# Kernel optimization log

Hardware: AMD Instinct MI355X
Metric: run time of the kernel (lower is better)

## Reference

```python
import jax, jax.numpy as jnp
import numpy as np


def _eta(pos, conj):
    # e[0] = pos[:,1::2] repeated into even/odd cols; e[1] = (+/-)pos[:,0::2] likewise
    c = jnp.repeat(pos[:, 1::2], 2, axis=1)
    s = jnp.repeat(pos[:, 0::2], 2, axis=1)
    return jnp.stack([c, s if conj else -s])  # [2, N, d]


def setup_inputs() -> dict:
    key = jax.random.key(0)
    ks = jax.random.split(key, 8)
    B, N, d, H = 8, 4096, 128, 4
    s = 0.02
    return {
        "x": jax.random.normal(ks[0], (B, N, d), jnp.float32),
        "pos": jax.random.normal(ks[1], (N, d), jnp.float32),
        "W_lt": jax.random.normal(ks[2], (d, d), jnp.float32) * s,
        "W_phi": jax.random.normal(ks[3], (d * H, d), jnp.float32) * s,
        "b_phi": jnp.zeros((d * H,), jnp.float32),
        "W_c1": jax.random.normal(ks[4], (H, H), jnp.float32) * s,
        "b_c1": jnp.zeros((H,), jnp.float32),
        "W_c2": jax.random.normal(ks[5], (1, H), jnp.float32) * s,
        "b_c2": jnp.zeros((1,), jnp.float32),
        "ln_g": jnp.ones((d,), jnp.float32),
        "ln_b": jnp.zeros((d,), jnp.float32),
        "W_f1": jax.random.normal(ks[6], (d, d), jnp.float32) * s,
        "b_f1": jnp.zeros((d,), jnp.float32),
        "W_f2": jax.random.normal(ks[7], (d, d), jnp.float32) * s,
        "b_f2": jnp.zeros((d,), jnp.float32),
    }


def reference(x, pos, W_lt, W_phi, b_phi, W_c1, b_c1, W_c2, b_c2,
              ln_g, ln_b, W_f1, b_f1, W_f2, b_f2):
    B, N, d = x.shape
    H = W_phi.shape[0] // d
    x = x @ W_lt.T                                   # linear_trans (no bias)
    e = _eta(pos, False)                             # [2,N,d]
    xe = x[None] * e[:, None]                        # [2,B,N,d]
    # A = ones(N,N) - I  =>  A @ v == sum over nodes minus self
    f = xe.sum(axis=2, keepdims=True) - xe           # [2,B,N,d]
    f_norm = jnp.sqrt(f[0] ** 2 + f[1] ** 2)         # [B,N,d]
    phi = ((x + pos[None]) @ W_phi.T + b_phi).reshape(B, N, H, d)
    # ReLU1(|f| - phi): relu(min(1, f_norm - phi))
    res = jax.nn.relu(jnp.minimum(1.0, f_norm[:, :, None, :] - phi))  # [B,N,H,d]
    ce = _eta(pos, True)
    fec = f[0] * ce[0][None] - f[1] * ce[1][None]    # [B,N,d]
    rfe = res * fec[:, :, None, :]                   # [B,N,H,d]
    # inverse transform: (1/N) * (M @ A) with A symmetric => sum-minus-self over node dim
    inv = (rfe.sum(axis=1, keepdims=True) - rfe) / N  # [B,N,H,d]
    t = inv.transpose(0, 1, 3, 2)                    # [B,N,d,H]
    comb = (jax.nn.relu(t @ W_c1.T + b_c1) @ W_c2.T + b_c2)[..., 0]  # [B,N,d]
    m = x + comb
    mu = m.mean(-1, keepdims=True)
    var = ((m - mu) ** 2).mean(-1, keepdims=True)
    mn = (m - mu) * jax.lax.rsqrt(var + 1e-6) * ln_g + ln_b
    return jax.nn.relu(mn @ W_f1.T + b_f1) @ W_f2.T + b_f2
```

## Files before the change

kernel.cpp:

```cpp
#include <hip/hip_runtime.h>
#include <hip/hip_bf16.h>
#include <hip/hip_fp8.h>


#define DEV __device__ __forceinline__

typedef __attribute__((ext_vector_type(8))) short bf16x8;
typedef __attribute__((ext_vector_type(4))) float f32x4;

constexpr int Bb = 8, Nn = 4096;
constexpr int BN = Bb * Nn;
constexpr int LDP = 136;
constexpr int P8  = 144;

union U8 { ushort u[8]; uint4 v; };

static DEV ushort f2bf(float f) {
    __hip_bfloat16 h = __float2bfloat16(f);
    return *reinterpret_cast<unsigned short*>(&h);
}
static DEV float bf2f(ushort u) {
    return __bfloat162float(*reinterpret_cast<const __hip_bfloat16*>(&u));
}
static DEV unsigned char f2fp8(float f) {
    __hip_fp8_e4m3 q(f);
    return q.__x;
}
static DEV float fp82f(unsigned char u) {
    __hip_fp8_e4m3 q;
    q.__x = u;
    return (float)q;
}

template <int MODE>
__global__ __launch_bounds__(256) void k_mfma_gemm(
    const void* __restrict__ Xv, const float* __restrict__ W,
    const float* __restrict__ bias, const float* __restrict__ pos,
    ushort* __restrict__ outB, unsigned char* __restrict__ out8)
{
    __shared__ __align__(16) ushort xs[64 * LDP];
    __shared__ __align__(16) ushort wsl[128 * LDP];
    const int t = threadIdx.x;
    const int row0 = blockIdx.x * 64;
    const int jt = (MODE == 1) ? blockIdx.y : 0;

    if (MODE == 0) {
        const float* X = (const float*)Xv;
        #pragma unroll
        for (int i = 0; i < 4; ++i) {
            int e = t + i * 256, r = e >> 4, c = (e & 15) * 8;
            const float* p = X + (size_t)(row0 + r) * 128 + c;
            float4 a = *reinterpret_cast<const float4*>(p);
            float4 b = *reinterpret_cast<const float4*>(p + 4);
            U8 u;
            u.u[0] = f2bf(a.x); u.u[1] = f2bf(a.y); u.u[2] = f2bf(a.z); u.u[3] = f2bf(a.w);
            u.u[4] = f2bf(b.x); u.u[5] = f2bf(b.y); u.u[6] = f2bf(b.z); u.u[7] = f2bf(b.w);
            *reinterpret_cast<uint4*>(xs + r * LDP + c) = u.v;
        }
    } else {
        const ushort* X = (const ushort*)Xv;
        #pragma unroll
        for (int i = 0; i < 4; ++i) {
            int e = t + i * 256, r = e >> 4, c = (e & 15) * 8;
            U8 u;
            u.v = *reinterpret_cast<const uint4*>(X + (size_t)(row0 + r) * 128 + c);
            int n = (row0 + r) & (Nn - 1);
            const float* q = pos + (size_t)n * 128 + c;
            float4 pa = *reinterpret_cast<const float4*>(q);
            float4 pb = *reinterpret_cast<const float4*>(q + 4);
            u.u[0] = f2bf(bf2f(u.u[0]) + pa.x);
            u.u[1] = f2bf(bf2f(u.u[1]) + pa.y);
            u.u[2] = f2bf(bf2f(u.u[2]) + pa.z);
            u.u[3] = f2bf(bf2f(u.u[3]) + pa.w);
            u.u[4] = f2bf(bf2f(u.u[4]) + pb.x);
            u.u[5] = f2bf(bf2f(u.u[5]) + pb.y);
            u.u[6] = f2bf(bf2f(u.u[6]) + pb.z);
            u.u[7] = f2bf(bf2f(u.u[7]) + pb.w);
            *reinterpret_cast<uint4*>(xs + r * LDP + c) = u.v;
        }
    }
    {
        const float* Wt = W + (size_t)jt * 128 * 128;
        #pragma unroll
        for (int i = 0; i < 8; ++i) {
            int e = t + i * 256, r = e >> 4, c = (e & 15) * 8;
            const float* p = Wt + (size_t)r * 128 + c;
            float4 a = *reinterpret_cast<const float4*>(p);
            float4 b = *reinterpret_cast<const float4*>(p + 4);
            U8 u;
            u.u[0] = f2bf(a.x); u.u[1] = f2bf(a.y); u.u[2] = f2bf(a.z); u.u[3] = f2bf(a.w);
            u.u[4] = f2bf(b.x); u.u[5] = f2bf(b.y); u.u[6] = f2bf(b.z); u.u[7] = f2bf(b.w);
            *reinterpret_cast<uint4*>(wsl + r * LDP + c) = u.v;
        }
    }
    __syncthreads();

    const int w = t >> 6, l = t & 63;
    const int lr = l & 15;
    const int lk = (l >> 4) * 8;

    f32x4 acc[8];
    #pragma unroll
    for (int cf = 0; cf < 8; ++cf) acc[cf] = f32x4{0.f, 0.f, 0.f, 0.f};

    #pragma unroll
    for (int ks = 0; ks < 4; ++ks) {
        bf16x8 a = *reinterpret_cast<const bf16x8*>(xs + (w * 16 + lr) * LDP + ks * 32 + lk);
        #pragma unroll
        for (int cf = 0; cf < 8; ++cf) {
            bf16x8 b = *reinterpret_cast<const bf16x8*>(wsl + (cf * 16 + lr) * LDP + ks * 32 + lk);
            acc[cf] = __builtin_amdgcn_mfma_f32_16x16x32_bf16(a, b, acc[cf], 0, 0, 0);
        }
    }

    __syncthreads();

    if (MODE == 0) {
        #pragma unroll
        for (int cf = 0; cf < 8; ++cf) {
            int col = cf * 16 + lr;
            #pragma unroll
            for (int reg = 0; reg < 4; ++reg) {
                int rl = w * 16 + (l >> 4) * 4 + reg;
                xs[rl * LDP + col] = f2bf(acc[cf][reg]);
            }
        }
        __syncthreads();
        #pragma unroll
        for (int i = 0; i < 4; ++i) {
            int e = t + i * 256, r = e >> 4, c = (e & 15) * 8;
            uint4 v = *reinterpret_cast<const uint4*>(xs + r * LDP + c);
            *reinterpret_cast<uint4*>(outB + (size_t)(row0 + r) * 128 + c) = v;
        }
    } else {
        unsigned char* x8 = reinterpret_cast<unsigned char*>(xs);
        #pragma unroll
        for (int cf = 0; cf < 8; ++cf) {
            int col = cf * 16 + lr;
            float bv = bias[jt * 128 + col];
            #pragma unroll
            for (int reg = 0; reg < 4; ++reg) {
                int rl = w * 16 + (l >> 4) * 4 + reg;
                x8[rl * P8 + col] = f2fp8(acc[cf][reg] + bv);
            }
        }
        __syncthreads();
        #pragma unroll
        for (int i = 0; i < 2; ++i) {
            int e = t + i * 256, r = e >> 3, c = (e & 7) * 16;
            uint4 v = *reinterpret_cast<const uint4*>(x8 + r * P8 + c);
            *reinterpret_cast<uint4*>(out8 + (size_t)(row0 + r) * 512 + jt * 128 + c) = v;
        }
    }
}

__global__ __launch_bounds__(256) void k_reduceS(
    const ushort* __restrict__ x1b, const float* __restrict__ pos,
    float* __restrict__ PS)
{
    int b = blockIdx.x >> 6, c64 = blockIdx.x & 63;
    int rr = threadIdx.x >> 5, d0 = (threadIdx.x & 31) * 4;
    float a0[4] = {0,0,0,0}, a1[4] = {0,0,0,0};
    #pragma unroll
    for (int i = 0; i < 8; ++i) {
        int n = c64 * 64 + i * 8 + rr;
        size_t r = (size_t)b * Nn + n;
        ushort4 xv = *reinterpret_cast<const ushort4*>(x1b + r * 128 + d0);
        float4 p = *reinterpret_cast<const float4*>(pos + (size_t)n * 128 + d0);
        float x0 = bf2f(xv.x), x1 = bf2f(xv.y), x2 = bf2f(xv.z), x3 = bf2f(xv.w);
        a0[0] += x0 * p.y; a1[0] += x0 * p.x;
        a0[1] += x1 * p.y; a1[1] += x1 * p.x;
        a0[2] += x2 * p.w; a1[2] += x2 * p.z;
        a0[3] += x3 * p.w; a1[3] += x3 * p.z;
    }
    __shared__ float redA[8][128], redB[8][128];
    #pragma unroll
    for (int j = 0; j < 4; ++j) { redA[rr][d0 + j] = a0[j]; redB[rr][d0 + j] = a1[j]; }
    __syncthreads();
    int tt = threadIdx.x;
    float s = 0.f;
    if (tt < 128) {
        #pragma unroll
        for (int k = 0; k < 8; ++k) s += redA[k][tt];
    } else {
        #pragma unroll
        for (int k = 0; k < 8; ++k) s += redB[k][tt - 128];
    }
    PS[(size_t)blockIdx.x * 256 + tt] = s;
}

__global__ __launch_bounds__(256) void k_finS(
    const float* __restrict__ PS, float* __restrict__ S0, float* __restrict__ S1)
{
    int b = blockIdx.x, t = threadIdx.x;
    float s = 0.f;
    #pragma unroll 8
    for (int c = 0; c < 64; ++c) s += PS[(size_t)(b * 64 + c) * 256 + t];
    if (t < 128) S0[b * 128 + t] = s;
    else         S1[b * 128 + (t - 128)] = s;
}

__global__ __launch_bounds__(256) void k_reduceT(
    const ushort* __restrict__ x1b, const unsigned char* __restrict__ phi8,
    const float* __restrict__ pos, const float* __restrict__ S0,
    const float* __restrict__ S1, float* __restrict__ PT)
{
    int b = blockIdx.x >> 6, c64 = blockIdx.x & 63;
    int rr = threadIdx.x >> 5, d0 = (threadIdx.x & 31) * 4;
    float4 S0v = *reinterpret_cast<const float4*>(S0 + b * 128 + d0);
    float4 S1v = *reinterpret_cast<const float4*>(S1 + b * 128 + d0);
    float S0a[4] = {S0v.x, S0v.y, S0v.z, S0v.w};
    float S1a[4] = {S1v.x, S1v.y, S1v.z, S1v.w};
    float acc[4][4];
    #pragma unroll
    for (int h = 0; h < 4; ++h)
        #pragma unroll
        for (int j = 0; j < 4; ++j) acc[h][j] = 0.f;

    #pragma unroll 2
    for (int i = 0; i < 8; ++i) {
        int n = c64 * 64 + i * 8 + rr;
        size_t r = (size_t)b * Nn + n;
        ushort4 xv4 = *reinterpret_cast<const ushort4*>(x1b + r * 128 + d0);
        float4 p = *reinterpret_cast<const float4*>(pos + (size_t)n * 128 + d0);
        float xv[4] = {bf2f(xv4.x), bf2f(xv4.y), bf2f(xv4.z), bf2f(xv4.w)};
        float cc[4] = {p.y, p.y, p.w, p.w};
        float ss[4] = {p.x, p.x, p.z, p.z};
        float fec[4], fn[4];
        #pragma unroll
        for (int j = 0; j < 4; ++j) {
            float f0 = S0a[j] - xv[j] * cc[j];
            float f1 = xv[j] * ss[j] - S1a[j];
            fn[j] = sqrtf(f0 * f0 + f1 * f1);
            fec[j] = f0 * cc[j] - f1 * ss[j];
        }
        #pragma unroll
        for (int h = 0; h < 4; ++h) {
            uchar4 ph4 = *reinterpret_cast<const uchar4*>(phi8 + r * 512 + h * 128 + d0);
            float ph[4] = {fp82f(ph4.x), fp82f(ph4.y), fp82f(ph4.z), fp82f(ph4.w)};
            #pragma unroll
            for (int j = 0; j < 4; ++j)
                acc[h][j] += fmaxf(0.f, fminf(1.f, fn[j] - ph[j])) * fec[j];
        }
    }
    __shared__ float red[8][512];
    #pragma unroll
    for (int h = 0; h < 4; ++h)
        #pragma unroll
        for (int j = 0; j < 4; ++j) red[rr][h * 128 + d0 + j] = acc[h][j];
    __syncthreads();
    int tt = threadIdx.x;
    #pragma unroll
    for (int q = 0; q < 2; ++q) {
        int idx = tt + q * 256;
        float s = 0.f;
        #pragma unroll
        for (int k = 0; k < 8; ++k) s += red[k][idx];
        PT[(size_t)blockIdx.x * 512 + idx] = s;
    }
}

__global__ __launch_bounds__(256) void k_finT(
    const float* __restrict__ PT, float* __restrict__ T)
{
    int idx = blockIdx.x * 256 + threadIdx.x;
    int b = idx >> 9, lo = idx & 511;
    float s = 0.f;
    #pragma unroll 8
    for (int c = 0; c < 64; ++c) s += PT[(size_t)b * 32768 + c * 512 + lo];
    T[idx] = s;
}

__global__ __launch_bounds__(256) void k_comb_ffn(
    const ushort* __restrict__ x1b, const unsigned char* __restrict__ phi8,
    const float* __restrict__ pos, const float* __restrict__ S0,
    const float* __restrict__ S1, const float* __restrict__ T,
    const float* __restrict__ Wc1, const float* __restrict__ bc1,
    const float* __restrict__ Wc2, const float* __restrict__ bc2,
    const float* __restrict__ lng, const float* __restrict__ lnb,
    const float* __restrict__ Wf1, const float* __restrict__ bf1,
    const float* __restrict__ Wf2, const float* __restrict__ bf2,
    float* __restrict__ out)
{
    __shared__ __align__(16) ushort xs[64 * LDP];
    __shared__ __align__(16) ushort wsl[128 * LDP];
    const int t = threadIdx.x;
    const int row0 = blockIdx.x * 64;
    const int w = t >> 6, l = t & 63;

    #pragma unroll
    for (int i = 0; i < 8; ++i) {
        int e = t + i * 256, r = e >> 4, c = (e & 15) * 8;
        const float* p = Wf1 + (size_t)r * 128 + c;
        float4 a = *reinterpret_cast<const float4*>(p);
        float4 b = *reinterpret_cast<const float4*>(p + 4);
        U8 u;
        u.u[0] = f2bf(a.x); u.u[1] = f2bf(a.y); u.u[2] = f2bf(a.z); u.u[3] = f2bf(a.w);
        u.u[4] = f2bf(b.x); u.u[5] = f2bf(b.y); u.u[6] = f2bf(b.z); u.u[7] = f2bf(b.w);
        *reinterpret_cast<uint4*>(wsl + r * LDP + c) = u.v;
    }

    {
        const int d0 = 2 * l;
        const float g0 = lng[d0], g1 = lng[d0 + 1];
        const float be0 = lnb[d0], be1 = lnb[d0 + 1];
        const float c20 = Wc2[0], c21 = Wc2[1], c22 = Wc2[2], c23 = Wc2[3];
        const float b2v = bc2[0];
        for (int i = 0; i < 16; ++i) {
            int rl = w * 16 + i;
            int rrow = row0 + rl;
            int b = rrow >> 12;
            int n = rrow & 4095;
            size_t r = (size_t)rrow;

            ushort2 xv2 = *reinterpret_cast<const ushort2*>(x1b + r * 128 + d0);
            float2 p2 = *reinterpret_cast<const float2*>(pos + (size_t)n * 128 + d0);
            float2 s0 = *reinterpret_cast<const float2*>(S0 + b * 128 + d0);
            float2 s1 = *reinterpret_cast<const float2*>(S1 + b * 128 + d0);
            float cc = p2.y, ss = p2.x;
            float xv[2] = {bf2f(xv2.x), bf2f(xv2.y)};
            float S0a[2] = {s0.x, s0.y}, S1a[2] = {s1.x, s1.y};
            float2 Tv[4];
            #pragma unroll
            for (int h = 0; h < 4; ++h)
                Tv[h] = *reinterpret_cast<const float2*>(T + (b * 4 + h) * 128 + d0);
            uchar2 ph2[4];
            #pragma unroll
            for (int h = 0; h < 4; ++h)
                ph2[h] = *reinterpret_cast<const uchar2*>(phi8 + r * 512 + h * 128 + d0);

            float m[2];
            #pragma unroll
            for (int q = 0; q < 2; ++q) {
                float f0 = S0a[q] - xv[q] * cc;
                float f1 = xv[q] * ss - S1a[q];
                float fn = sqrtf(f0 * f0 + f1 * f1);
                float fec = f0 * cc - f1 * ss;
                float inv[4];
                #pragma unroll
                for (int h = 0; h < 4; ++h) {
                    float ph = fp82f(q ? ph2[h].y : ph2[h].x);
                    float res = fmaxf(0.f, fminf(1.f, fn - ph));
                    float tv = q ? Tv[h].y : Tv[h].x;
                    inv[h] = (tv - res * fec) * (1.f / (float)Nn);
                }
                float comb = b2v;
                float wc2a[4] = {c20, c21, c22, c23};
                #pragma unroll
                for (int h = 0; h < 4; ++h) {
                    float u = bc1[h];
                    #pragma unroll
                    for (int h2 = 0; h2 < 4; ++h2) u += Wc1[h * 4 + h2] * inv[h2];
                    comb += fmaxf(u, 0.f) * wc2a[h];
                }
                m[q] = xv[q] + comb;
            }

            float s = m[0] + m[1];
            #pragma unroll
            for (int off = 32; off; off >>= 1) s += __shfl_xor(s, off);
            float mu = s * (1.f / 128.f);
            float e0 = m[0] - mu, e1 = m[1] - mu;
            float v = e0 * e0 + e1 * e1;
            #pragma unroll
            for (int off = 32; off; off >>= 1) v += __shfl_xor(v, off);
            float rstd = rsqrtf(v * (1.f / 128.f) + 1e-6f);
            ushort2 o;
            o.x = f2bf(e0 * rstd * g0 + be0);
            o.y = f2bf(e1 * rstd * g1 + be1);
            *reinterpret_cast<ushort2*>(xs + rl * LDP + d0) = o;
        }
    }
    __syncthreads();

    const int lr = l & 15;
    const int lk = (l >> 4) * 8;

    f32x4 acc[8];
    #pragma unroll
    for (int cf = 0; cf < 8; ++cf) acc[cf] = f32x4{0.f, 0.f, 0.f, 0.f};
    #pragma unroll
    for (int ks = 0; ks < 4; ++ks) {
        bf16x8 a = *reinterpret_cast<const bf16x8*>(xs + (w * 16 + lr) * LDP + ks * 32 + lk);
        #pragma unroll
        for (int cf = 0; cf < 8; ++cf) {
            bf16x8 b = *reinterpret_cast<const bf16x8*>(wsl + (cf * 16 + lr) * LDP + ks * 32 + lk);
            acc[cf] = __builtin_amdgcn_mfma_f32_16x16x32_bf16(a, b, acc[cf], 0, 0, 0);
        }
    }
    __syncthreads();

    #pragma unroll
    for (int cf = 0; cf < 8; ++cf) {
        int col = cf * 16 + lr;
        float bv = bf1[col];
        #pragma unroll
        for (int reg = 0; reg < 4; ++reg) {
            int rl = w * 16 + (l >> 4) * 4 + reg;
            xs[rl * LDP + col] = f2bf(fmaxf(acc[cf][reg] + bv, 0.f));
        }
    }
    #pragma unroll
    for (int i = 0; i < 8; ++i) {
        int e = t + i * 256, r = e >> 4, c = (e & 15) * 8;
        const float* p = Wf2 + (size_t)r * 128 + c;
        float4 a = *reinterpret_cast<const float4*>(p);
        float4 b = *reinterpret_cast<const float4*>(p + 4);
        U8 u;
        u.u[0] = f2bf(a.x); u.u[1] = f2bf(a.y); u.u[2] = f2bf(a.z); u.u[3] = f2bf(a.w);
        u.u[4] = f2bf(b.x); u.u[5] = f2bf(b.y); u.u[6] = f2bf(b.z); u.u[7] = f2bf(b.w);
        *reinterpret_cast<uint4*>(wsl + r * LDP + c) = u.v;
    }
    __syncthreads();

    #pragma unroll
    for (int cf = 0; cf < 8; ++cf) acc[cf] = f32x4{0.f, 0.f, 0.f, 0.f};
    #pragma unroll
    for (int ks = 0; ks < 4; ++ks) {
        bf16x8 a = *reinterpret_cast<const bf16x8*>(xs + (w * 16 + lr) * LDP + ks * 32 + lk);
        #pragma unroll
        for (int cf = 0; cf < 8; ++cf) {
            bf16x8 b = *reinterpret_cast<const bf16x8*>(wsl + (cf * 16 + lr) * LDP + ks * 32 + lk);
            acc[cf] = __builtin_amdgcn_mfma_f32_16x16x32_bf16(a, b, acc[cf], 0, 0, 0);
        }
    }
    #pragma unroll
    for (int cf = 0; cf < 8; ++cf) {
        int col = cf * 16 + lr;
        float bv = bf2[col];
        #pragma unroll
        for (int reg = 0; reg < 4; ++reg) {
            int r = row0 + w * 16 + (l >> 4) * 4 + reg;
            out[(size_t)r * 128 + col] = acc[cf][reg] + bv;
        }
    }
}

extern "C" void kernel_launch(void* const* d_in, const int* in_sizes, int n_in,
                              void* d_out, int out_size, void* d_ws, size_t ws_size,
                              hipStream_t stream)
{
    const float* x    = (const float*)d_in[0];
    const float* pos  = (const float*)d_in[1];
    const float* Wlt  = (const float*)d_in[2];
    const float* Wphi = (const float*)d_in[3];
    const float* bphi = (const float*)d_in[4];
    const float* Wc1  = (const float*)d_in[5];
    const float* bc1  = (const float*)d_in[6];
    const float* Wc2  = (const float*)d_in[7];
    const float* bc2  = (const float*)d_in[8];
    const float* lng  = (const float*)d_in[9];
    const float* lnb  = (const float*)d_in[10];
    const float* Wf1  = (const float*)d_in[11];
    const float* bf1  = (const float*)d_in[12];
    const float* Wf2  = (const float*)d_in[13];
    const float* bf2  = (const float*)d_in[14];

    float* ws = (float*)d_ws;
    ushort* x1b = (ushort*)ws;
    float* S0   = ws + 2097152;
    float* S1   = S0 + 1024;
    float* T    = S1 + 1024;
    float* PS   = T + 4096;
    float* PT   = PS + 131072;
    unsigned char* phi8 = (unsigned char*)(ws + 2496512);
    float* out  = (float*)d_out;

    k_mfma_gemm<0><<<dim3(BN / 64), 256, 0, stream>>>(x, Wlt, nullptr, pos, x1b, nullptr);
    k_reduceS<<<dim3(512), 256, 0, stream>>>(x1b, pos, PS);
    k_finS<<<dim3(Bb), 256, 0, stream>>>(PS, S0, S1);
    k_mfma_gemm<1><<<dim3(BN / 64, 4), 256, 0, stream>>>(x1b, Wphi, bphi, pos, nullptr, phi8);
    k_reduceT<<<dim3(512), 256, 0, stream>>>(x1b, phi8, pos, S0, S1, PT);
    k_finT<<<dim3(16), 256, 0, stream>>>(PT, T);
    k_comb_ffn<<<dim3(BN / 64), 256, 0, stream>>>(x1b, phi8, pos, S0, S1, T,
                                                  Wc1, bc1, Wc2, bc2, lng, lnb,
                                                  Wf1, bf1, Wf2, bf2, out);
}
```

Baseline: 73.61 us.

## Fuse S-reduction into first GEMM and loop phi GEMM over head tiles

Merges the partial S reduction into the first GEMM's epilogue so x1b is reduced straight from LDS instead of being re-read from global memory, which removes one kernel launch. The phi GEMM now loops over the four 128-column weight tiles inside one block, so the x+pos tile is loaded and converted once rather than four times. The store of each fp8 tile overlaps with loading the next weight tile. FP8 conversions switch from the hip_fp8 header to the raw cvt builtins. In exchange, the grid for the phi GEMM shrinks 4x, with 512 blocks that each run a serial loop, and the partial-sum grid changes from 512 to 512 blocks with a different row grouping. Both could lower parallelism and occupancy because the kernels now use more LDS.

```diff
diff --git a/kernel.cpp b/kernel.cpp
--- a/kernel.cpp
+++ b/kernel.cpp
@@ -1,6 +1,5 @@
 #include <hip/hip_runtime.h>
 #include <hip/hip_bf16.h>
-#include <hip/hip_fp8.h>
 
 
 #define DEV __device__ __forceinline__
@@ -23,75 +22,42 @@
     return __bfloat162float(*reinterpret_cast<const __hip_bfloat16*>(&u));
 }
 static DEV unsigned char f2fp8(float f) {
-    __hip_fp8_e4m3 q(f);
-    return q.__x;
-}
-static DEV float fp82f(unsigned char u) {
-    __hip_fp8_e4m3 q;
-    q.__x = u;
-    return (float)q;
-}
-
-template <int MODE>
-__global__ __launch_bounds__(256) void k_mfma_gemm(
-    const void* __restrict__ Xv, const float* __restrict__ W,
-    const float* __restrict__ bias, const float* __restrict__ pos,
-    ushort* __restrict__ outB, unsigned char* __restrict__ out8)
+    return (unsigned char)(__builtin_amdgcn_cvt_pk_fp8_f32(f, f, 0u, false) & 0xff);
+}
+static DEV float fp8lo(unsigned int u, int) ;
+
+__global__ __launch_bounds__(256) void k_gemm0(
+    const float* __restrict__ X, const float* __restrict__ W,
+    const float* __restrict__ pos, ushort* __restrict__ x1b,
+    float* __restrict__ PS)
 {
     __shared__ __align__(16) ushort xs[64 * LDP];
     __shared__ __align__(16) ushort wsl[128 * LDP];
+    __shared__ float red[4][2][128];
     const int t = threadIdx.x;
     const int row0 = blockIdx.x * 64;
-    const int jt = (MODE == 1) ? blockIdx.y : 0;
-
-    if (MODE == 0) {
-        const float* X = (const float*)Xv;
-        #pragma unroll
-        for (int i = 0; i < 4; ++i) {
-            int e = t + i * 256, r = e >> 4, c = (e & 15) * 8;
-            const float* p = X + (size_t)(row0 + r) * 128 + c;
-            float4 a = *reinterpret_cast<const float4*>(p);
-            float4 b = *reinterpret_cast<const float4*>(p + 4);
-            U8 u;
-            u.u[0] = f2bf(a.x); u.u[1] = f2bf(a.y); u.u[2] = f2bf(a.z); u.u[3] = f2bf(a.w);
-            u.u[4] = f2bf(b.x); u.u[5] = f2bf(b.y); u.u[6] = f2bf(b.z); u.u[7] = f2bf(b.w);
-            *reinterpret_cast<uint4*>(xs + r * LDP + c) = u.v;
-        }
-    } else {
-        const ushort* X = (const ushort*)Xv;
-        #pragma unroll
-        for (int i = 0; i < 4; ++i) {
-            int e = t + i * 256, r = e >> 4, c = (e & 15) * 8;
-            U8 u;
-            u.v = *reinterpret_cast<const uint4*>(X + (size_t)(row0 + r) * 128 + c);
-            int n = (row0 + r) & (Nn - 1);
-            const float* q = pos + (size_t)n * 128 + c;
-            float4 pa = *reinterpret_cast<const float4*>(q);
-            float4 pb = *reinterpret_cast<const float4*>(q + 4);
-            u.u[0] = f2bf(bf2f(u.u[0]) + pa.x);
-            u.u[1] = f2bf(bf2f(u.u[1]) + pa.y);
-            u.u[2] = f2bf(bf2f(u.u[2]) + pa.z);
-            u.u[3] = f2bf(bf2f(u.u[3]) + pa.w);
-            u.u[4] = f2bf(bf2f(u.u[4]) + pb.x);
-            u.u[5] = f2bf(bf2f(u.u[5]) + pb.y);
-            u.u[6] = f2bf(bf2f(u.u[6]) + pb.z);
-            u.u[7] = f2bf(bf2f(u.u[7]) + pb.w);
-            *reinterpret_cast<uint4*>(xs + r * LDP + c) = u.v;
-        }
-    }
-    {
-        const float* Wt = W + (size_t)jt * 128 * 128;
-        #pragma unroll
-        for (int i = 0; i < 8; ++i) {
-            int e = t + i * 256, r = e >> 4, c = (e & 15) * 8;
-            const float* p = Wt + (size_t)r * 128 + c;
-            float4 a = *reinterpret_cast<const float4*>(p);
-            float4 b = *reinterpret_cast<const float4*>(p + 4);
-            U8 u;
-            u.u[0] = f2bf(a.x); u.u[1] = f2bf(a.y); u.u[2] = f2bf(a.z); u.u[3] = f2bf(a.w);
-            u.u[4] = f2bf(b.x); u.u[5] = f2bf(b.y); u.u[6] = f2bf(b.z); u.u[7] = f2bf(b.w);
-            *reinterpret_cast<uint4*>(wsl + r * LDP + c) = u.v;
-        }
+
+    #pragma unroll
+    for (int i = 0; i < 4; ++i) {
+        int e = t + i * 256, r = e >> 4, c = (e & 15) * 8;
+        const float* p = X + (size_t)(row0 + r) * 128 + c;
+        float4 a = *reinterpret_cast<const float4*>(p);
+        float4 b = *reinterpret_cast<const float4*>(p + 4);
+        U8 u;
+        u.u[0] = f2bf(a.x); u.u[1] = f2bf(a.y); u.u[2] = f2bf(a.z); u.u[3] = f2bf(a.w);
+        u.u[4] = f2bf(b.x); u.u[5] = f2bf(b.y); u.u[6] = f2bf(b.z); u.u[7] = f2bf(b.w);
+        *reinterpret_cast<uint4*>(xs + r * LDP + c) = u.v;
+    }
+    #pragma unroll
+    for (int i = 0; i < 8; ++i) {
+        int e = t + i * 256, r = e >> 4, c = (e & 15) * 8;
+        const float* p = W + (size_t)r * 128 + c;
+        float4 a = *reinterpret_cast<const float4*>(p);
+        float4 b = *reinterpret_cast<const float4*>(p + 4);
+        U8 u;
+        u.u[0] = f2bf(a.x); u.u[1] = f2bf(a.y); u.u[2] = f2bf(a.z); u.u[3] = f2bf(a.w);
+        u.u[4] = f2bf(b.x); u.u[5] = f2bf(b.y); u.u[6] = f2bf(b.z); u.u[7] = f2bf(b.w);
+        *reinterpret_cast<uint4*>(wsl + r * LDP + c) = u.v;
     }
     __syncthreads();
 
@@ -102,7 +68,6 @@
     f32x4 acc[8];
     #pragma unroll
     for (int cf = 0; cf < 8; ++cf) acc[cf] = f32x4{0.f, 0.f, 0.f, 0.f};
-
     #pragma unroll
     for (int ks = 0; ks < 4; ++ks) {
         bf16x8 a = *reinterpret_cast<const bf16x8*>(xs + (w * 16 + lr) * LDP + ks * 32 + lk);
@@ -112,81 +77,49 @@
             acc[cf] = __builtin_amdgcn_mfma_f32_16x16x32_bf16(a, b, acc[cf], 0, 0, 0);
         }
     }
-
-    __syncthreads();
-
-    if (MODE == 0) {
-        #pragma unroll
-        for (int cf = 0; cf < 8; ++cf) {
-            int col = cf * 16 + lr;
-            #pragma unroll
-            for (int reg = 0; reg < 4; ++reg) {
-                int rl = w * 16 + (l >> 4) * 4 + reg;
-                xs[rl * LDP + col] = f2bf(acc[cf][reg]);
-            }
-        }
-        __syncthreads();
-        #pragma unroll
-        for (int i = 0; i < 4; ++i) {
-            int e = t + i * 256, r = e >> 4, c = (e & 15) * 8;
-            uint4 v = *reinterpret_cast<const uint4*>(xs + r * LDP + c);
-            *reinterpret_cast<uint4*>(outB + (size_t)(row0 + r) * 128 + c) = v;
-        }
-    } else {
-        unsigned char* x8 = reinterpret_cast<unsigned char*>(xs);
-        #pragma unroll
-        for (int cf = 0; cf < 8; ++cf) {
-            int col = cf * 16 + lr;
-            float bv = bias[jt * 128 + col];
-            #pragma unroll
-            for (int reg = 0; reg < 4; ++reg) {
-                int rl = w * 16 + (l >> 4) * 4 + reg;
-                x8[rl * P8 + col] = f2fp8(acc[cf][reg] + bv);
-            }
-        }
-        __syncthreads();
-        #pragma unroll
-        for (int i = 0; i < 2; ++i) {
-            int e = t + i * 256, r = e >> 3, c = (e & 7) * 16;
-            uint4 v = *reinterpret_cast<const uint4*>(x8 + r * P8 + c);
-            *reinterpret_cast<uint4*>(out8 + (size_t)(row0 + r) * 512 + jt * 128 + c) = v;
-        }
-    }
-}
-
-__global__ __launch_bounds__(256) void k_reduceS(
-    const ushort* __restrict__ x1b, const float* __restrict__ pos,
-    float* __restrict__ PS)
-{
-    int b = blockIdx.x >> 6, c64 = blockIdx.x & 63;
-    int rr = threadIdx.x >> 5, d0 = (threadIdx.x & 31) * 4;
-    float a0[4] = {0,0,0,0}, a1[4] = {0,0,0,0};
-    #pragma unroll
-    for (int i = 0; i < 8; ++i) {
-        int n = c64 * 64 + i * 8 + rr;
-        size_t r = (size_t)b * Nn + n;
-        ushort4 xv = *reinterpret_cast<const ushort4*>(x1b + r * 128 + d0);
-        float4 p = *reinterpret_cast<const float4*>(pos + (size_t)n * 128 + d0);
-        float x0 = bf2f(xv.x), x1 = bf2f(xv.y), x2 = bf2f(xv.z), x3 = bf2f(xv.w);
-        a0[0] += x0 * p.y; a1[0] += x0 * p.x;
-        a0[1] += x1 * p.y; a1[1] += x1 * p.x;
-        a0[2] += x2 * p.w; a1[2] += x2 * p.z;
-        a0[3] += x3 * p.w; a1[3] += x3 * p.z;
-    }
-    __shared__ float redA[8][128], redB[8][128];
-    #pragma unroll
-    for (int j = 0; j < 4; ++j) { redA[rr][d0 + j] = a0[j]; redB[rr][d0 + j] = a1[j]; }
-    __syncthreads();
-    int tt = threadIdx.x;
-    float s = 0.f;
-    if (tt < 128) {
-        #pragma unroll
-        for (int k = 0; k < 8; ++k) s += redA[k][tt];
-    } else {
-        #pragma unroll
-        for (int k = 0; k < 8; ++k) s += redB[k][tt - 128];
-    }
-    PS[(size_t)blockIdx.x * 256 + tt] = s;
+    __syncthreads();
+
+    #pragma unroll
+    for (int cf = 0; cf < 8; ++cf) {
+        int col = cf * 16 + lr;
+        #pragma unroll
+        for (int reg = 0; reg < 4; ++reg) {
+            int rl = w * 16 + (l >> 4) * 4 + reg;
+            xs[rl * LDP + col] = f2bf(acc[cf][reg]);
+        }
+    }
+    __syncthreads();
+
+    #pragma unroll
+    for (int i = 0; i < 4; ++i) {
+        int e = t + i * 256, r = e >> 4, c = (e & 15) * 8;
+        uint4 v = *reinterpret_cast<const uint4*>(xs + r * LDP + c);
+        *reinterpret_cast<uint4*>(x1b + (size_t)(row0 + r) * 128 + c) = v;
+    }
+
+    {
+        int c2 = t & 63, g = t >> 6;
+        float a0e = 0.f, a1e = 0.f, a0o = 0.f, a1o = 0.f;
+        #pragma unroll 4
+        for (int i = 0; i < 16; ++i) {
+            int r = g * 16 + i;
+            int n = (row0 + r) & (Nn - 1);
+            unsigned int v = *reinterpret_cast<const unsigned int*>(xs + r * LDP + 2 * c2);
+            float lo = bf2f((ushort)(v & 0xffff));
+            float hi = bf2f((ushort)(v >> 16));
+            float2 p = *reinterpret_cast<const float2*>(pos + (size_t)n * 128 + 2 * c2);
+            a0e += lo * p.y; a1e += lo * p.x;
+            a0o += hi * p.y; a1o += hi * p.x;
+        }
+        red[g][0][2 * c2] = a0e; red[g][0][2 * c2 + 1] = a0o;
+        red[g][1][2 * c2] = a1e; red[g][1][2 * c2 + 1] = a1o;
+    }
+    __syncthreads();
+    {
+        int half = t >> 7, col = t & 127;
+        float s = red[0][half][col] + red[1][half][col] + red[2][half][col] + red[3][half][col];
+        PS[(size_t)blockIdx.x * 256 + t] = s;
+    }
 }
 
 __global__ __launch_bounds__(256) void k_finS(
@@ -198,6 +131,98 @@
     for (int c = 0; c < 64; ++c) s += PS[(size_t)(b * 64 + c) * 256 + t];
     if (t < 128) S0[b * 128 + t] = s;
     else         S1[b * 128 + (t - 128)] = s;
+}
+
+__global__ __launch_bounds__(256) void k_gemm_phi(
+    const ushort* __restrict__ x1b, const float* __restrict__ W,
+    const float* __restrict__ bias, const float* __restrict__ pos,
+    unsigned char* __restrict__ phi8)
+{
+    __shared__ __align__(16) ushort xs[64 * LDP];
+    __shared__ __align__(16) ushort wsl[128 * LDP];
+    __shared__ __align__(16) unsigned char p8[64 * P8];
+    const int t = threadIdx.x;
+    const int row0 = blockIdx.x * 64;
+    const int w = t >> 6, l = t & 63;
+    const int lr = l & 15;
+    const int lk = (l >> 4) * 8;
+
+    #pragma unroll
+    for (int i = 0; i < 4; ++i) {
+        int e = t + i * 256, r = e >> 4, c = (e & 15) * 8;
+        U8 u;
+        u.v = *reinterpret_cast<const uint4*>(x1b + (size_t)(row0 + r) * 128 + c);
+        int n = (row0 + r) & (Nn - 1);
+        const float* q = pos + (size_t)n * 128 + c;
+        float4 pa = *reinterpret_cast<const float4*>(q);
+        float4 pb = *reinterpret_cast<const float4*>(q + 4);
+        u.u[0] = f2bf(bf2f(u.u[0]) + pa.x);
+        u.u[1] = f2bf(bf2f(u.u[1]) + pa.y);
+        u.u[2] = f2bf(bf2f(u.u[2]) + pa.z);
+        u.u[3] = f2bf(bf2f(u.u[3]) + pa.w);
+        u.u[4] = f2bf(bf2f(u.u[4]) + pb.x);
+        u.u[5] = f2bf(bf2f(u.u[5]) + pb.y);
+        u.u[6] = f2bf(bf2f(u.u[6]) + pb.z);
+        u.u[7] = f2bf(bf2f(u.u[7]) + pb.w);
+        *reinterpret_cast<uint4*>(xs + r * LDP + c) = u.v;
+    }
+
+    for (int jt = 0; jt < 4; ++jt) {
+        __syncthreads();
+        {
+            const float* Wt = W + (size_t)jt * 128 * 128;
+            #pragma unroll
+            for (int i = 0; i < 8; ++i) {
+                int e = t + i * 256, r = e >> 4, c = (e & 15) * 8;
+                const float* p = Wt + (size_t)r * 128 + c;
+                float4 a = *reinterpret_cast<const float4*>(p);
+                float4 b = *reinterpret_cast<const float4*>(p + 4);
+                U8 u;
+                u.u[0] = f2bf(a.x); u.u[1] = f2bf(a.y); u.u[2] = f2bf(a.z); u.u[3] = f2bf(a.w);
+                u.u[4] = f2bf(b.x); u.u[5] = f2bf(b.y); u.u[6] = f2bf(b.z); u.u[7] = f2bf(b.w);
+                *reinterpret_cast<uint4*>(wsl + r * LDP + c) = u.v;
+            }
+            if (jt > 0) {
+                #pragma unroll
+                for (int i = 0; i < 2; ++i) {
+                    int e = t + i * 256, r = e >> 3, c = (e & 7) * 16;
+                    uint4 v = *reinterpret_cast<const uint4*>(p8 + r * P8 + c);
+                    *reinterpret_cast<uint4*>(phi8 + (size_t)(row0 + r) * 512 + (jt - 1) * 128 + c) = v;
+                }
+            }
+        }
+        __syncthreads();
+
+        f32x4 acc[8];
+        #pragma unroll
+        for (int cf = 0; cf < 8; ++cf) acc[cf] = f32x4{0.f, 0.f, 0.f, 0.f};
+        #pragma unroll
+        for (int ks = 0; ks < 4; ++ks) {
+            bf16x8 a = *reinterpret_cast<const bf16x8*>(xs + (w * 16 + lr) * LDP + ks * 32 + lk);
+            #pragma unroll
+            for (int cf = 0; cf < 8; ++cf) {
+                bf16x8 b = *reinterpret_cast<const bf16x8*>(wsl + (cf * 16 + lr) * LDP + ks * 32 + lk);
+                acc[cf] = __builtin_amdgcn_mfma_f32_16x16x32_bf16(a, b, acc[cf], 0, 0, 0);
+            }
+        }
+        #pragma unroll
+        for (int cf = 0; cf < 8; ++cf) {
+            int col = cf * 16 + lr;
+            float bv = bias[jt * 128 + col];
+            #pragma unroll
+            for (int reg = 0; reg < 4; ++reg) {
+                int rl = w * 16 + (l >> 4) * 4 + reg;
+                p8[rl * P8 + col] = f2fp8(acc[cf][reg] + bv);
+            }
+        }
+    }
+    __syncthreads();
+    #pragma unroll
+    for (int i = 0; i < 2; ++i) {
+        int e = t + i * 256, r = e >> 3, c = (e & 7) * 16;
+        uint4 v = *reinterpret_cast<const uint4*>(p8 + r * P8 + c);
+        *reinterpret_cast<uint4*>(phi8 + (size_t)(row0 + r) * 512 + 3 * 128 + c) = v;
+    }
 }
 
 __global__ __launch_bounds__(256) void k_reduceT(
@@ -236,11 +261,15 @@
         }
         #pragma unroll
         for (int h = 0; h < 4; ++h) {
-            uchar4 ph4 = *reinterpret_cast<const uchar4*>(phi8 + r * 512 + h * 128 + d0);
-            float ph[4] = {fp82f(ph4.x), fp82f(ph4.y), fp82f(ph4.z), fp82f(ph4.w)};
-            #pragma unroll
-            for (int j = 0; j < 4; ++j)
-                acc[h][j] += fmaxf(0.f, fminf(1.f, fn[j] - ph[j])) * fec[j];
+            unsigned int pv = *reinterpret_cast<const unsigned int*>(phi8 + r * 512 + h * 128 + d0);
+            float ph0 = __builtin_amdgcn_cvt_f32_fp8(pv, 0);
+            float ph1 = __builtin_amdgcn_cvt_f32_fp8(pv, 1);
+            float ph2 = __builtin_amdgcn_cvt_f32_fp8(pv, 2);
+            float ph3 = __builtin_amdgcn_cvt_f32_fp8(pv, 3);
+            acc[h][0] += fmaxf(0.f, fminf(1.f, fn[0] - ph0)) * fec[0];
+            acc[h][1] += fmaxf(0.f, fminf(1.f, fn[1] - ph1)) * fec[1];
+            acc[h][2] += fmaxf(0.f, fminf(1.f, fn[2] - ph2)) * fec[2];
+            acc[h][3] += fmaxf(0.f, fminf(1.f, fn[3] - ph3)) * fec[3];
         }
     }
     __shared__ float red[8][512];
@@ -304,7 +333,7 @@
         const int d0 = 2 * l;
         const float g0 = lng[d0], g1 = lng[d0 + 1];
         const float be0 = lnb[d0], be1 = lnb[d0 + 1];
-        const float c20 = Wc2[0], c21 = Wc2[1], c22 = Wc2[2], c23 = Wc2[3];
+        const float c2v[4] = {Wc2[0], Wc2[1], Wc2[2], Wc2[3]};
         const float b2v = bc2[0];
         for (int i = 0; i < 16; ++i) {
             int rl = w * 16 + i;
@@ -324,10 +353,13 @@
             #pragma unroll
             for (int h = 0; h < 4; ++h)
                 Tv[h] = *reinterpret_cast<const float2*>(T + (b * 4 + h) * 128 + d0);
-            uchar2 ph2[4];
-            #pragma unroll
-            for (int h = 0; h < 4; ++h)
-                ph2[h] = *reinterpret_cast<const uchar2*>(phi8 + r * 512 + h * 128 + d0);
+            float phv[4][2];
+            #pragma unroll
+            for (int h = 0; h < 4; ++h) {
+                unsigned int pu = *reinterpret_cast<const ushort*>(phi8 + r * 512 + h * 128 + d0);
+                phv[h][0] = __builtin_amdgcn_cvt_f32_fp8(pu, 0);
+                phv[h][1] = __builtin_amdgcn_cvt_f32_fp8(pu, 1);
+            }
 
             float m[2];
             #pragma unroll
@@ -339,19 +371,17 @@
                 float inv[4];
                 #pragma unroll
                 for (int h = 0; h < 4; ++h) {
-                    float ph = fp82f(q ? ph2[h].y : ph2[h].x);
-                    float res = fmaxf(0.f, fminf(1.f, fn - ph));
+                    float res = fmaxf(0.f, fminf(1.f, fn - phv[h][q]));
                     float tv = q ? Tv[h].y : Tv[h].x;
                     inv[h] = (tv - res * fec) * (1.f / (float)Nn);
                 }
                 float comb = b2v;
-                float wc2a[4] = {c20, c21, c22, c23};
                 #pragma unroll
                 for (int h = 0; h < 4; ++h) {
                     float u = bc1[h];
                     #pragma unroll
                     for (int h2 = 0; h2 < 4; ++h2) u += Wc1[h * 4 + h2] * inv[h2];
-                    comb += fmaxf(u, 0.f) * wc2a[h];
+                    comb += fmaxf(u, 0.f) * c2v[h];
                 }
                 m[q] = xv[q] + comb;
             }
@@ -466,10 +496,9 @@
     unsigned char* phi8 = (unsigned char*)(ws + 2496512);
     float* out  = (float*)d_out;
 
-    k_mfma_gemm<0><<<dim3(BN / 64), 256, 0, stream>>>(x, Wlt, nullptr, pos, x1b, nullptr);
-    k_reduceS<<<dim3(512), 256, 0, stream>>>(x1b, pos, PS);
+    k_gemm0<<<dim3(BN / 64), 256, 0, stream>>>(x, Wlt, pos, x1b, PS);
     k_finS<<<dim3(Bb), 256, 0, stream>>>(PS, S0, S1);
-    k_mfma_gemm<1><<<dim3(BN / 64, 4), 256, 0, stream>>>(x1b, Wphi, bphi, pos, nullptr, phi8);
+    k_gemm_phi<<<dim3(BN / 64), 256, 0, stream>>>(x1b, Wphi, bphi, pos, phi8);
     k_reduceT<<<dim3(512), 256, 0, stream>>>(x1b, phi8, pos, S0, S1, PT);
     k_finT<<<dim3(16), 256, 0, stream>>>(PT, T);
     k_comb_ffn<<<dim3(BN / 64), 256, 0, stream>>>(x1b, phi8, pos, S0, S1, T,
```

Result: no change. 72.65 us (-1.3%).
